# Performance work log

Hardware: AMD Instinct MI355X
Metric: run time of the kernel (lower is better)

The kernel has to match this reference:

```python
import jax, jax.numpy as jnp
import numpy as np

D_MODEL = 1024
B, S = 4, 4096


def setup_inputs() -> dict:
    key = jax.random.key(0)
    k1, k2, k3, k4, k5 = jax.random.split(key, 5)
    lim = 1.0 / np.sqrt(D_MODEL)  # nn.Linear default init range
    x = jax.random.normal(k1, (B, S, D_MODEL), dtype=jnp.float32)
    mask = jnp.ones((B, S), dtype=jnp.float32)
    W_up = jax.random.uniform(k2, (D_MODEL, D_MODEL), jnp.float32, -lim, lim)
    b_up = jax.random.uniform(k3, (D_MODEL,), jnp.float32, -lim, lim)
    W_f = jax.random.uniform(k4, (D_MODEL, D_MODEL), jnp.float32, -lim, lim)
    b_f = jax.random.uniform(k5, (D_MODEL,), jnp.float32, -lim, lim)
    decay_param = jnp.zeros((1,), dtype=jnp.float32)
    return {"x": x, "mask": mask, "W_up": W_up, "b_up": b_up,
            "W_f": W_f, "b_f": b_f, "decay_param": decay_param}


def _decay_scan(u, decay):
    # h_t = decay * h_{t-1} + u_t  along axis=1, via associative scan.
    # Element: (a, b) representing h -> a*h + b; compose: (a1*a2, b1*a2 + b2).
    a = jnp.broadcast_to(decay, u.shape)

    def combine(c1, c2):
        a1, b1 = c1
        a2, b2 = c2
        return a1 * a2, b1 * a2 + b2

    _, h = jax.lax.associative_scan(combine, (a, u), axis=1)
    return h


def reference(x, mask, W_up, b_up, W_f, b_f, decay_param):
    decay = jax.nn.sigmoid(decay_param)[0]
    # u_i = mask_i * linear_update(x_i)
    u = (jnp.einsum('bsd,ed->bse', x, W_up) + b_up) * mask[..., None]
    # h_t = sum_{i<=t} decay^(t-i) * u_i  (exponential-decay recurrence)
    h = _decay_scan(u, decay)
    return jnp.einsum('bsd,ed->bse', h, W_f) + b_f
```

## Files before the change

kernel.cpp:

```cpp
#include <hip/hip_runtime.h>
#include <hip/hip_bf16.h>
#include <cstdint>
#include <cstddef>

#define DMODEL 1024
#define BATCH  4
#define SEQ    4096
#define BSROWS (BATCH*SEQ)
#define CHUNK  32
#define NCHUNK (SEQ/CHUNK)
#define NCH_T  (BATCH*NCHUNK)

typedef __attribute__((ext_vector_type(8))) short bf16x8;
typedef __attribute__((ext_vector_type(4))) float f32x4;


__device__ __forceinline__ unsigned short f2bf(float f) {
  union { float f; uint32_t u; } v; v.f = f;
  uint32_t u = v.u;
  u += 0x7FFFu + ((u >> 16) & 1u);
  return (unsigned short)(u >> 16);
}

__device__ __forceinline__ float sigmoid_dev(const float* dp) {
  return 1.0f / (1.0f + expf(-dp[0]));
}

typedef __attribute__((address_space(1))) void void_g;
typedef __attribute__((address_space(3))) void void_l;

__device__ __forceinline__ void gl2lds16(const void* g, void* l) {
  __builtin_amdgcn_global_load_lds((void_g*)g, (void_l*)l, 16, 0, 0);
}

__device__ __forceinline__ void kloop64(
    const unsigned short* __restrict__ A, const unsigned short* __restrict__ B,
    int m0, int n0, f32x4 acc[2][2],
    unsigned short* As, unsigned short* Bs, int tid) {
  int lane = tid & 63, w = tid >> 6, wm = w & 1, wn = w >> 1;
  int quad = lane >> 4, l16 = lane & 15;
  int r = tid >> 3, cch = tid & 7;
  int g = cch ^ (r & 7);
  const bf16x8* Av = (const bf16x8*)As;
  const bf16x8* Bv = (const bf16x8*)Bs;
  for (int k0 = 0; k0 < DMODEL; k0 += 64) {
    gl2lds16(A + (size_t)(m0 + r) * DMODEL + k0 + g * 8,      As + r * 64 + cch * 8);
    gl2lds16(A + (size_t)(m0 + 32 + r) * DMODEL + k0 + g * 8, As + (32 + r) * 64 + cch * 8);
    gl2lds16(B + (size_t)(n0 + r) * DMODEL + k0 + g * 8,      Bs + r * 64 + cch * 8);
    gl2lds16(B + (size_t)(n0 + 32 + r) * DMODEL + k0 + g * 8, Bs + (32 + r) * 64 + cch * 8);
    __syncthreads();
    #pragma unroll
    for (int kk = 0; kk < 2; ++kk) {
      bf16x8 af[2], bfr[2];
      #pragma unroll
      for (int i = 0; i < 2; ++i) {
        int rowA = wm * 32 + i * 16 + l16;
        af[i]  = Av[rowA * 8 + ((kk * 4 + quad) ^ (l16 & 7))];
        int rowB = wn * 32 + i * 16 + l16;
        bfr[i] = Bv[rowB * 8 + ((kk * 4 + quad) ^ (l16 & 7))];
      }
      #pragma unroll
      for (int i = 0; i < 2; ++i)
        #pragma unroll
        for (int j = 0; j < 2; ++j)
          acc[i][j] = __builtin_amdgcn_mfma_f32_16x16x32_bf16(af[i], bfr[j], acc[i][j], 0, 0, 0);
    }
    __syncthreads();
  }
}

__global__ __launch_bounds__(256) void prep_kernel(
    const float* __restrict__ x, const float* __restrict__ mask,
    const float* __restrict__ W_up, const float* __restrict__ b_up,
    const float* __restrict__ W_f, const float* __restrict__ dp,
    unsigned short* __restrict__ Wf_bf, unsigned short* __restrict__ WupT,
    float* __restrict__ bb, unsigned short* __restrict__ hv,
    float* __restrict__ carry, float* __restrict__ lbeta,
    float* __restrict__ cbeta) {
  __shared__ float tile[32][33];
  int blk = blockIdx.x;
  int tid = threadIdx.x;

  if (blk < 512) {
    float decay = sigmoid_dev(dp);
    int b = blk / NCHUNK, c = blk % NCHUNK;
    int base = b * SEQ + c * CHUNK;
    const float4* xp = (const float4*)(x + (size_t)base * DMODEL);
    const float4* mp4 = (const float4*)(mask + base);
    float mreg[32];
    #pragma unroll
    for (int q = 0; q < 8; ++q) {
      float4 t = mp4[q];
      mreg[q * 4 + 0] = t.x; mreg[q * 4 + 1] = t.y;
      mreg[q * 4 + 2] = t.z; mreg[q * 4 + 3] = t.w;
    }
    float4 h = make_float4(0.f, 0.f, 0.f, 0.f);
    #pragma unroll
    for (int s = 0; s < CHUNK; ++s) {
      float m = mreg[s];
      float4 xv = xp[(size_t)s * (DMODEL / 4) + tid];
      h.x = decay * h.x + m * xv.x;
      h.y = decay * h.y + m * xv.y;
      h.z = decay * h.z + m * xv.z;
      h.w = decay * h.w + m * xv.w;
      ushort4 o;
      o.x = f2bf(h.x); o.y = f2bf(h.y); o.z = f2bf(h.z); o.w = f2bf(h.w);
      ((ushort4*)hv)[(size_t)(base + s) * (DMODEL / 4) + tid] = o;
    }
    ((float4*)carry)[(size_t)blk * (DMODEL / 4) + tid] = h;
  } else if (blk < 1536) {
    int e = blk - 512;
    int lane = tid & 63, w = tid >> 6;
    float4 v = ((const float4*)(W_f + (size_t)e * DMODEL))[tid];
    float4 bu = ((const float4*)b_up)[tid];
    ushort4 o;
    o.x = f2bf(v.x); o.y = f2bf(v.y); o.z = f2bf(v.z); o.w = f2bf(v.w);
    ((ushort4*)(Wf_bf + (size_t)e * DMODEL))[tid] = o;
    float s = v.x * bu.x + v.y * bu.y + v.z * bu.z + v.w * bu.w;
    #pragma unroll
    for (int off = 32; off; off >>= 1) s += __shfl_down(s, off);
    if (lane == 0) ((float*)tile)[w] = s;
    __syncthreads();
    if (tid == 0)
      bb[e] = ((float*)tile)[0] + ((float*)tile)[1] +
              ((float*)tile)[2] + ((float*)tile)[3];
  } else if (blk < 2560) {
    int id = blk - 1536;
    int bx = id & 31, by = id >> 5;
    int tx = tid & 31, ty = tid >> 5;
    int xx = bx * 32 + tx;
    int y0 = by * 32;
    for (int j = ty; j < 32; j += 8)
      tile[j][tx] = W_up[(size_t)(y0 + j) * DMODEL + xx];
    __syncthreads();
    int ox = by * 32 + tx;
    int oy0 = bx * 32;
    for (int j = ty; j < 32; j += 8)
      WupT[(size_t)(oy0 + j) * DMODEL + ox] = f2bf(tile[tx][j]);
  } else {
    float decay = sigmoid_dev(dp);
    int t = (blk - 2560) * 256 + tid;
    int s = t & 31;
    int cbase = t & ~31;
    float hb = 0.f;
    for (int i = 0; i <= s; ++i)
      hb = decay * hb + mask[cbase + i];
    lbeta[t] = hb;
    if (s == 31) cbeta[t >> 5] = hb;
  }
}

__global__ __launch_bounds__(256) void mid2_kernel(
    const unsigned short* __restrict__ Wf_bf,
    const unsigned short* __restrict__ WupT,
    unsigned short* __restrict__ Wc,
    const float* __restrict__ carry, const float* __restrict__ cbeta,
    const float* __restrict__ dp,
    unsigned short* __restrict__ Pbf, float* __restrict__ pbeta) {
  __shared__ unsigned short As[64 * 64];
  __shared__ unsigned short Bs[64 * 64];
  int tid = threadIdx.x;
  if (blockIdx.x < 256) {
    int mt = blockIdx.x >> 4, nt = blockIdx.x & 15;
    f32x4 acc[2][2] = {};
    kloop64(Wf_bf, WupT, mt * 64, nt * 64, acc, As, Bs, tid);
    int lane = tid & 63, w = tid >> 6, wm = w & 1, wn = w >> 1;
    int quad = lane >> 4, l16 = lane & 15;
    #pragma unroll
    for (int j = 0; j < 2; ++j) {
      int col = nt * 64 + wn * 32 + j * 16 + l16;
      #pragma unroll
      for (int i = 0; i < 2; ++i) {
        int rowb = mt * 64 + wm * 32 + i * 16 + quad * 4;
        #pragma unroll
        for (int rr = 0; rr < 4; ++rr)
          Wc[(size_t)(rowb + rr) * DMODEL + col] = f2bf(acc[i][j][rr]);
      }
    }
  } else {
    float decay = sigmoid_dev(dp);
    float dL = powf(decay, (float)CHUNK);
    int gid = (blockIdx.x - 256) * 256 + tid;
    int b = gid >> 10, dd = gid & 1023;
    float P = 0.f;
    for (int c0 = 0; c0 < NCHUNK; c0 += 8) {
      float v[8];
      #pragma unroll
      for (int j = 0; j < 8; ++j)
        v[j] = carry[(size_t)(b * NCHUNK + c0 + j) * DMODEL + dd];
      #pragma unroll
      for (int j = 0; j < 8; ++j) {
        Pbf[(size_t)(b * NCHUNK + c0 + j) * DMODEL + dd] = f2bf(P);
        P = dL * P + v[j];
      }
    }
    if (dd == 0) {
      float Pb = 0.f;
      for (int c0 = 0; c0 < NCHUNK; c0 += 16) {
        float v[16];
        #pragma unroll
        for (int j = 0; j < 16; ++j) v[j] = cbeta[b * NCHUNK + c0 + j];
        #pragma unroll
        for (int j = 0; j < 16; ++j) {
          pbeta[b * NCHUNK + c0 + j] = Pb;
          Pb = dL * Pb + v[j];
        }
      }
    }
  }
}

__global__ __launch_bounds__(256) void pout_kernel(
    const unsigned short* __restrict__ Pbf,
    const unsigned short* __restrict__ Wc,
    const float* __restrict__ pbeta, const float* __restrict__ bb,
    float* __restrict__ Pout) {
  __shared__ unsigned short As[64 * 64];
  __shared__ unsigned short Bs[64 * 64];
  int tid = threadIdx.x;
  int mt = blockIdx.x >> 4, nt = blockIdx.x & 15;
  f32x4 acc[2][2] = {};
  kloop64(Pbf, Wc, mt * 64, nt * 64, acc, As, Bs, tid);
  int lane = tid & 63, w = tid >> 6, wm = w & 1, wn = w >> 1;
  int quad = lane >> 4, l16 = lane & 15;
  #pragma unroll
  for (int j = 0; j < 2; ++j) {
    int col = nt * 64 + wn * 32 + j * 16 + l16;
    float bbv = bb[col];
    #pragma unroll
    for (int i = 0; i < 2; ++i) {
      int rowb = mt * 64 + wm * 32 + i * 16 + quad * 4;
      #pragma unroll
      for (int rr = 0; rr < 4; ++rr) {
        int row = rowb + rr;
        Pout[(size_t)row * DMODEL + col] = acc[i][j][rr] + pbeta[row] * bbv;
      }
    }
  }
}

__global__ __launch_bounds__(256) void gemm_main(
    const unsigned short* __restrict__ A,
    const unsigned short* __restrict__ Bm,
    const float* __restrict__ Pout,
    const float* __restrict__ lbeta,
    const float* __restrict__ bb,
    const float* __restrict__ bias_f,
    const float* __restrict__ dp,
    float* __restrict__ out) {
  __shared__ unsigned short As[128 * 32];
  __shared__ unsigned short Bs[128 * 32];
  __shared__ float dpow[CHUNK];
  int tid = threadIdx.x;
  if (tid < CHUNK) {
    float decay = sigmoid_dev(dp);
    dpow[tid] = powf(decay, (float)(tid + 1));
  }
  int lane = tid & 63, w = tid >> 6, wm = w & 1, wn = w >> 1;
  int quad = lane >> 4, l16 = lane & 15;
  int r = tid >> 2;
  int c4 = tid & 3;
  int g = c4 ^ ((r >> 1) & 3);
  int phi = (l16 >> 1) & 3;
  int m0 = (blockIdx.x & 127) * 128;
  int n0 = (blockIdx.x >> 7) * 128;
  f32x4 acc[4][4] = {};
  const bf16x8* Av = (const bf16x8*)As;
  const bf16x8* Bv = (const bf16x8*)Bs;
  for (int k0 = 0; k0 < DMODEL; k0 += 32) {
    gl2lds16(A + (size_t)(m0 + r) * DMODEL + k0 + g * 8,        As + r * 32 + c4 * 8);
    gl2lds16(A + (size_t)(m0 + 64 + r) * DMODEL + k0 + g * 8,   As + (64 + r) * 32 + c4 * 8);
    gl2lds16(Bm + (size_t)(n0 + r) * DMODEL + k0 + g * 8,       Bs + r * 32 + c4 * 8);
    gl2lds16(Bm + (size_t)(n0 + 64 + r) * DMODEL + k0 + g * 8,  Bs + (64 + r) * 32 + c4 * 8);
    __syncthreads();
    bf16x8 af[4], bfr[4];
    #pragma unroll
    for (int i = 0; i < 4; ++i) {
      int rowA = wm * 64 + i * 16 + l16;
      af[i]  = Av[rowA * 4 + (quad ^ phi)];
      int rowB = wn * 64 + i * 16 + l16;
      bfr[i] = Bv[rowB * 4 + (quad ^ phi)];
    }
    #pragma unroll
    for (int i = 0; i < 4; ++i)
      #pragma unroll
      for (int j = 0; j < 4; ++j)
        acc[i][j] = __builtin_amdgcn_mfma_f32_16x16x32_bf16(af[i], bfr[j], acc[i][j], 0, 0, 0);
    __syncthreads();
  }
  #pragma unroll
  for (int j = 0; j < 4; ++j) {
    int col = n0 + wn * 64 + j * 16 + l16;
    float bbv = bb[col];
    float bfv = bias_f[col];
    #pragma unroll
    for (int i = 0; i < 4; ++i) {
      int rowb = m0 + wm * 64 + i * 16 + quad * 4;
      #pragma unroll
      for (int rr = 0; rr < 4; ++rr) {
        int row = rowb + rr;
        float po = Pout[(size_t)(row >> 5) * DMODEL + col];
        out[(size_t)row * DMODEL + col] =
            acc[i][j][rr] + dpow[row & 31] * po + lbeta[row] * bbv + bfv;
      }
    }
  }
}


extern "C" void kernel_launch(void* const* d_in, const int* in_sizes, int n_in,
                              void* d_out, int out_size, void* d_ws, size_t ws_size,
                              hipStream_t stream) {
  const float* x    = (const float*)d_in[0];
  const float* mask = (const float*)d_in[1];
  const float* W_up = (const float*)d_in[2];
  const float* b_up = (const float*)d_in[3];
  const float* W_f  = (const float*)d_in[4];
  const float* b_f  = (const float*)d_in[5];
  const float* dp   = (const float*)d_in[6];
  float* out = (float*)d_out;

  char* ws = (char*)d_ws;
  unsigned short* hv    = (unsigned short*)(ws);
  unsigned short* Wc    = (unsigned short*)(ws + 33554432);
  unsigned short* Wf_bf = (unsigned short*)(ws + 35651584);
  unsigned short* WupT  = (unsigned short*)(ws + 37748736);
  float* carry  = (float*)(ws + 39845888);
  unsigned short* Pbf = (unsigned short*)(ws + 41943040);
  float* Pout   = (float*)(ws + 42991616);
  float* lbeta  = (float*)(ws + 45088768);
  float* cbeta  = (float*)(ws + 45154304);
  float* pbeta  = (float*)(ws + 45156352);
  float* bb     = (float*)(ws + 45158400);

  prep_kernel<<<2624, 256, 0, stream>>>(x, mask, W_up, b_up, W_f, dp,
                                        Wf_bf, WupT, bb, hv, carry, lbeta, cbeta);
  mid2_kernel<<<272, 256, 0, stream>>>(Wf_bf, WupT, Wc, carry, cbeta, dp,
                                       Pbf, pbeta);
  pout_kernel<<<128, 256, 0, stream>>>(Pbf, Wc, pbeta, bb, Pout);
  gemm_main<<<1024, 256, 0, stream>>>(hv, Wc, Pout, lbeta, bb, b_f, dp, out);
}
```

Baseline: 203.5 us.

## Merge prep, mid and pout kernels into one cooperative kernel with grid syncs

```diff
diff --git a/kernel.cpp b/kernel.cpp
--- a/kernel.cpp
+++ b/kernel.cpp
@@ -1,7 +1,10 @@
 #include <hip/hip_runtime.h>
+#include <hip/hip_cooperative_groups.h>
 #include <hip/hip_bf16.h>
 #include <cstdint>
 #include <cstddef>
+
+namespace cg = cooperative_groups;
 
 #define DMODEL 1024
 #define BATCH  4
@@ -69,99 +72,91 @@
   }
 }
 
-__global__ __launch_bounds__(256) void prep_kernel(
+__global__ __launch_bounds__(256) void fused_pre(
     const float* __restrict__ x, const float* __restrict__ mask,
     const float* __restrict__ W_up, const float* __restrict__ b_up,
     const float* __restrict__ W_f, const float* __restrict__ dp,
     unsigned short* __restrict__ Wf_bf, unsigned short* __restrict__ WupT,
     float* __restrict__ bb, unsigned short* __restrict__ hv,
     float* __restrict__ carry, float* __restrict__ lbeta,
-    float* __restrict__ cbeta) {
-  __shared__ float tile[32][33];
+    float* __restrict__ cbeta, unsigned short* __restrict__ Wc,
+    unsigned short* __restrict__ Pbf, float* __restrict__ pbeta,
+    float* __restrict__ Pout) {
+  cg::grid_group grid = cg::this_grid();
+  __shared__ unsigned short As[64 * 64];
+  __shared__ unsigned short Bs[64 * 64];
   int blk = blockIdx.x;
   int tid = threadIdx.x;
 
-  if (blk < 512) {
-    float decay = sigmoid_dev(dp);
-    int b = blk / NCHUNK, c = blk % NCHUNK;
-    int base = b * SEQ + c * CHUNK;
-    const float4* xp = (const float4*)(x + (size_t)base * DMODEL);
-    const float4* mp4 = (const float4*)(mask + base);
-    float mreg[32];
-    #pragma unroll
-    for (int q = 0; q < 8; ++q) {
-      float4 t = mp4[q];
-      mreg[q * 4 + 0] = t.x; mreg[q * 4 + 1] = t.y;
-      mreg[q * 4 + 2] = t.z; mreg[q * 4 + 3] = t.w;
-    }
-    float4 h = make_float4(0.f, 0.f, 0.f, 0.f);
-    #pragma unroll
-    for (int s = 0; s < CHUNK; ++s) {
-      float m = mreg[s];
-      float4 xv = xp[(size_t)s * (DMODEL / 4) + tid];
-      h.x = decay * h.x + m * xv.x;
-      h.y = decay * h.y + m * xv.y;
-      h.z = decay * h.z + m * xv.z;
-      h.w = decay * h.w + m * xv.w;
+  for (int item = blk; item < 2624; item += 512) {
+    if (item < 512) {
+      float decay = sigmoid_dev(dp);
+      int b = item / NCHUNK, c = item % NCHUNK;
+      int base = b * SEQ + c * CHUNK;
+      const float4* xp = (const float4*)(x + (size_t)base * DMODEL);
+      const float* mp = mask + base;
+      float4 h = make_float4(0.f, 0.f, 0.f, 0.f);
+      #pragma unroll 8
+      for (int s = 0; s < CHUNK; ++s) {
+        float m = mp[s];
+        float4 xv = xp[(size_t)s * (DMODEL / 4) + tid];
+        h.x = decay * h.x + m * xv.x;
+        h.y = decay * h.y + m * xv.y;
+        h.z = decay * h.z + m * xv.z;
+        h.w = decay * h.w + m * xv.w;
+        ushort4 o;
+        o.x = f2bf(h.x); o.y = f2bf(h.y); o.z = f2bf(h.z); o.w = f2bf(h.w);
+        ((ushort4*)hv)[(size_t)(base + s) * (DMODEL / 4) + tid] = o;
+      }
+      ((float4*)carry)[(size_t)item * (DMODEL / 4) + tid] = h;
+    } else if (item < 1536) {
+      int e = item - 512;
+      int lane = tid & 63, w = tid >> 6;
+      float* red = (float*)Bs;
+      float4 v = ((const float4*)(W_f + (size_t)e * DMODEL))[tid];
+      float4 bu = ((const float4*)b_up)[tid];
       ushort4 o;
-      o.x = f2bf(h.x); o.y = f2bf(h.y); o.z = f2bf(h.z); o.w = f2bf(h.w);
-      ((ushort4*)hv)[(size_t)(base + s) * (DMODEL / 4) + tid] = o;
-    }
-    ((float4*)carry)[(size_t)blk * (DMODEL / 4) + tid] = h;
-  } else if (blk < 1536) {
-    int e = blk - 512;
-    int lane = tid & 63, w = tid >> 6;
-    float4 v = ((const float4*)(W_f + (size_t)e * DMODEL))[tid];
-    float4 bu = ((const float4*)b_up)[tid];
-    ushort4 o;
-    o.x = f2bf(v.x); o.y = f2bf(v.y); o.z = f2bf(v.z); o.w = f2bf(v.w);
-    ((ushort4*)(Wf_bf + (size_t)e * DMODEL))[tid] = o;
-    float s = v.x * bu.x + v.y * bu.y + v.z * bu.z + v.w * bu.w;
-    #pragma unroll
-    for (int off = 32; off; off >>= 1) s += __shfl_down(s, off);
-    if (lane == 0) ((float*)tile)[w] = s;
-    __syncthreads();
-    if (tid == 0)
-      bb[e] = ((float*)tile)[0] + ((float*)tile)[1] +
-              ((float*)tile)[2] + ((float*)tile)[3];
-  } else if (blk < 2560) {
-    int id = blk - 1536;
-    int bx = id & 31, by = id >> 5;
-    int tx = tid & 31, ty = tid >> 5;
-    int xx = bx * 32 + tx;
-    int y0 = by * 32;
-    for (int j = ty; j < 32; j += 8)
-      tile[j][tx] = W_up[(size_t)(y0 + j) * DMODEL + xx];
-    __syncthreads();
-    int ox = by * 32 + tx;
-    int oy0 = bx * 32;
-    for (int j = ty; j < 32; j += 8)
-      WupT[(size_t)(oy0 + j) * DMODEL + ox] = f2bf(tile[tx][j]);
-  } else {
-    float decay = sigmoid_dev(dp);
-    int t = (blk - 2560) * 256 + tid;
-    int s = t & 31;
-    int cbase = t & ~31;
-    float hb = 0.f;
-    for (int i = 0; i <= s; ++i)
-      hb = decay * hb + mask[cbase + i];
-    lbeta[t] = hb;
-    if (s == 31) cbeta[t >> 5] = hb;
-  }
-}
-
-__global__ __launch_bounds__(256) void mid2_kernel(
-    const unsigned short* __restrict__ Wf_bf,
-    const unsigned short* __restrict__ WupT,
-    unsigned short* __restrict__ Wc,
-    const float* __restrict__ carry, const float* __restrict__ cbeta,
-    const float* __restrict__ dp,
-    unsigned short* __restrict__ Pbf, float* __restrict__ pbeta) {
-  __shared__ unsigned short As[64 * 64];
-  __shared__ unsigned short Bs[64 * 64];
-  int tid = threadIdx.x;
-  if (blockIdx.x < 256) {
-    int mt = blockIdx.x >> 4, nt = blockIdx.x & 15;
+      o.x = f2bf(v.x); o.y = f2bf(v.y); o.z = f2bf(v.z); o.w = f2bf(v.w);
+      ((ushort4*)(Wf_bf + (size_t)e * DMODEL))[tid] = o;
+      float s = v.x * bu.x + v.y * bu.y + v.z * bu.z + v.w * bu.w;
+      #pragma unroll
+      for (int off = 32; off; off >>= 1) s += __shfl_down(s, off);
+      if (lane == 0) red[w] = s;
+      __syncthreads();
+      if (tid == 0) bb[e] = red[0] + red[1] + red[2] + red[3];
+      __syncthreads();
+    } else if (item < 2560) {
+      float (*tile)[33] = (float(*)[33])As;
+      int id = item - 1536;
+      int bx = id & 31, by = id >> 5;
+      int tx = tid & 31, ty = tid >> 5;
+      int xx = bx * 32 + tx;
+      int y0 = by * 32;
+      for (int j = ty; j < 32; j += 8)
+        tile[j][tx] = W_up[(size_t)(y0 + j) * DMODEL + xx];
+      __syncthreads();
+      int ox = by * 32 + tx;
+      int oy0 = bx * 32;
+      for (int j = ty; j < 32; j += 8)
+        WupT[(size_t)(oy0 + j) * DMODEL + ox] = f2bf(tile[tx][j]);
+      __syncthreads();
+    } else {
+      float decay = sigmoid_dev(dp);
+      int t = (item - 2560) * 256 + tid;
+      int s = t & 31;
+      int cbase = t & ~31;
+      float hb = 0.f;
+      for (int i = 0; i <= s; ++i)
+        hb = decay * hb + mask[cbase + i];
+      lbeta[t] = hb;
+      if (s == 31) cbeta[t >> 5] = hb;
+    }
+  }
+
+  grid.sync();
+
+  if (blk < 256) {
+    int mt = blk >> 4, nt = blk & 15;
     f32x4 acc[2][2] = {};
     kloop64(Wf_bf, WupT, mt * 64, nt * 64, acc, As, Bs, tid);
     int lane = tid & 63, w = tid >> 6, wm = w & 1, wn = w >> 1;
@@ -177,10 +172,10 @@
           Wc[(size_t)(rowb + rr) * DMODEL + col] = f2bf(acc[i][j][rr]);
       }
     }
-  } else {
+  } else if (blk < 272) {
     float decay = sigmoid_dev(dp);
     float dL = powf(decay, (float)CHUNK);
-    int gid = (blockIdx.x - 256) * 256 + tid;
+    int gid = (blk - 256) * 256 + tid;
     int b = gid >> 10, dd = gid & 1023;
     float P = 0.f;
     for (int c0 = 0; c0 < NCHUNK; c0 += 8) {
@@ -208,32 +203,27 @@
       }
     }
   }
-}
-
-__global__ __launch_bounds__(256) void pout_kernel(
-    const unsigned short* __restrict__ Pbf,
-    const unsigned short* __restrict__ Wc,
-    const float* __restrict__ pbeta, const float* __restrict__ bb,
-    float* __restrict__ Pout) {
-  __shared__ unsigned short As[64 * 64];
-  __shared__ unsigned short Bs[64 * 64];
-  int tid = threadIdx.x;
-  int mt = blockIdx.x >> 4, nt = blockIdx.x & 15;
-  f32x4 acc[2][2] = {};
-  kloop64(Pbf, Wc, mt * 64, nt * 64, acc, As, Bs, tid);
-  int lane = tid & 63, w = tid >> 6, wm = w & 1, wn = w >> 1;
-  int quad = lane >> 4, l16 = lane & 15;
-  #pragma unroll
-  for (int j = 0; j < 2; ++j) {
-    int col = nt * 64 + wn * 32 + j * 16 + l16;
-    float bbv = bb[col];
-    #pragma unroll
-    for (int i = 0; i < 2; ++i) {
-      int rowb = mt * 64 + wm * 32 + i * 16 + quad * 4;
-      #pragma unroll
-      for (int rr = 0; rr < 4; ++rr) {
-        int row = rowb + rr;
-        Pout[(size_t)row * DMODEL + col] = acc[i][j][rr] + pbeta[row] * bbv;
+
+  grid.sync();
+
+  if (blk < 128) {
+    int mt = blk >> 4, nt = blk & 15;
+    f32x4 acc[2][2] = {};
+    kloop64(Pbf, Wc, mt * 64, nt * 64, acc, As, Bs, tid);
+    int lane = tid & 63, w = tid >> 6, wm = w & 1, wn = w >> 1;
+    int quad = lane >> 4, l16 = lane & 15;
+    #pragma unroll
+    for (int j = 0; j < 2; ++j) {
+      int col = nt * 64 + wn * 32 + j * 16 + l16;
+      float bbv = bb[col];
+      #pragma unroll
+      for (int i = 0; i < 2; ++i) {
+        int rowb = mt * 64 + wm * 32 + i * 16 + quad * 4;
+        #pragma unroll
+        for (int rr = 0; rr < 4; ++rr) {
+          int row = rowb + rr;
+          Pout[(size_t)row * DMODEL + col] = acc[i][j][rr] + pbeta[row] * bbv;
+        }
       }
     }
   }
@@ -333,10 +323,13 @@
   float* pbeta  = (float*)(ws + 45156352);
   float* bb     = (float*)(ws + 45158400);
 
-  prep_kernel<<<2624, 256, 0, stream>>>(x, mask, W_up, b_up, W_f, dp,
-                                        Wf_bf, WupT, bb, hv, carry, lbeta, cbeta);
-  mid2_kernel<<<272, 256, 0, stream>>>(Wf_bf, WupT, Wc, carry, cbeta, dp,
-                                       Pbf, pbeta);
-  pout_kernel<<<128, 256, 0, stream>>>(Pbf, Wc, pbeta, bb, Pout);
+  void* cargs[] = {
+    (void*)&x, (void*)&mask, (void*)&W_up, (void*)&b_up, (void*)&W_f,
+    (void*)&dp, (void*)&Wf_bf, (void*)&WupT, (void*)&bb, (void*)&hv,
+    (void*)&carry, (void*)&lbeta, (void*)&cbeta, (void*)&Wc, (void*)&Pbf,
+    (void*)&pbeta, (void*)&Pout
+  };
+  hipLaunchCooperativeKernel((void*)fused_pre, dim3(512), dim3(256),
+                             cargs, 0, stream);
   gemm_main<<<1024, 256, 0, stream>>>(hv, Wc, Pout, lbeta, bb, b_f, dp, out);
 }
```

Result: slower. 347.1 us (+70.6%).
